# Kernel tuning notes

Hardware: AMD Instinct MI355X
Metric: run time of the kernel (lower is better)

Reference implementation:

```python
import jax, jax.numpy as jnp
import numpy as np


def _seg_softmax(e, seg, n):
    m = jax.ops.segment_max(e, seg, num_segments=n)
    ex = jnp.exp(e - m[seg])
    s = jax.ops.segment_sum(ex, seg, num_segments=n)
    return ex / (s[seg] + 1e-16)


def _gat_conv(x, src, dst, ea, W, a_s, a_d, We, a_e, b, heads, C, concat, N):
    # PyG GATConv math (eval mode, no dropout)
    h = (x @ W).reshape(N, heads, C)                    # [N,H,C]
    he = (ea @ We).reshape(-1, heads, C)                # [Ef,H,C]
    al = jnp.sum(h * a_s, -1)[src] + jnp.sum(h * a_d, -1)[dst] + jnp.sum(he * a_e, -1)
    al = jax.nn.leaky_relu(al, 0.2)                     # [Ef,H]
    alpha = _seg_softmax(al, dst, N)
    out = jax.ops.segment_sum(alpha[:, :, None] * h[src], dst, num_segments=N)
    out = out.reshape(N, heads * C) if concat else out.mean(1)
    return out + b


def _ln(x, g, b):
    mu = x.mean(-1, keepdims=True)
    v = x.var(-1, keepdims=True)
    return (x - mu) / jnp.sqrt(v + 1e-5) * g + b


def setup_inputs() -> dict:
    key = jax.random.key(0)
    ks = jax.random.split(key, 20)
    B, L, E_PER = 512, 64, 4
    N = B * L
    E = N * E_PER
    x = jax.random.normal(ks[0], (N, 55), jnp.float32)
    # within-graph random edges (each graph is a contiguous block of L nodes)
    off = (jnp.arange(E) // (L * E_PER)) * L
    src = off + jax.random.randint(ks[1], (E,), 0, L)
    dst = off + jax.random.randint(ks[2], (E,), 0, L)
    edge_index = jnp.stack([src, dst])
    edge_attr = jax.random.uniform(ks[3], (E, 6), dtype=jnp.float32)
    node_gid = jnp.arange(N) // L
    food_ids = jax.random.randint(ks[4], (B,), 0, 29)
    p = lambda i, shape: jax.random.normal(ks[i], shape, jnp.float32) * 0.05
    return dict(
        x=x, edge_attr=edge_attr, edge_index=edge_index, node_gid=node_gid, food_ids=food_ids,
        W1=p(5, (55, 1024)), as1=p(6, (4, 256)), ad1=p(7, (4, 256)),
        We1=p(8, (6, 1024)), ae1=p(9, (4, 256)), b1=jnp.zeros((1024,), jnp.float32),
        g1=jnp.ones((1024,), jnp.float32), be1=jnp.zeros((1024,), jnp.float32),
        W2=p(10, (1024, 256)), as2=p(11, (1, 256)), ad2=p(12, (1, 256)),
        We2=p(13, (6, 256)), ae2=p(14, (1, 256)), b2=jnp.zeros((256,), jnp.float32),
        g2=jnp.ones((256,), jnp.float32), be2=jnp.zeros((256,), jnp.float32),
        Wa=p(15, (256, 256)), va=p(16, (256,)), emb=p(17, (29, 256)))


def reference(x, edge_attr, edge_index, node_gid, food_ids,
              W1, as1, ad1, We1, ae1, b1, g1, be1,
              W2, as2, ad2, We2, ae2, b2, g2, be2,
              Wa, va, emb):
    N = x.shape[0]
    B = food_ids.shape[0]
    src, dst = edge_index[0], edge_index[1]
    # add self loops; self-loop edge_attr = mean of incoming edge attrs (PyG fill_value='mean')
    ones = jnp.ones((src.shape[0],), x.dtype)
    deg = jax.ops.segment_sum(ones, dst, num_segments=N)
    mean_ea = jax.ops.segment_sum(edge_attr, dst, num_segments=N) / jnp.maximum(deg, 1.0)[:, None]
    loop = jnp.arange(N)
    src_f = jnp.concatenate([src, loop])
    dst_f = jnp.concatenate([dst, loop])
    ea_f = jnp.concatenate([edge_attr, mean_ea], 0)
    # GATEncoder
    h = _gat_conv(x, src_f, dst_f, ea_f, W1, as1, ad1, We1, ae1, b1, 4, 256, True, N)
    h = jax.nn.relu(_ln(h, g1, be1))
    h = _gat_conv(h, src_f, dst_f, ea_f, W2, as2, ad2, We2, ae2, b2, 1, 256, False, N)
    h = _ln(h, g2, be2)                                  # [N,256]
    # per-graph attention over nodes, then attention-weighted max-pool
    scores = jnp.tanh(h @ Wa) @ va                       # [N]
    attn = _seg_softmax(scores, node_gid, B)             # [N]
    hw = h * attn[:, None]
    drug_fea = jax.ops.segment_max(hw, node_gid, num_segments=B)[:, None, :]  # [B,1,256]
    food_fea = emb[food_ids][:, None, :]                 # [B,1,256]
    return drug_fea, food_fea, attn
```

## Files before the change

kernel.cpp:

```cpp
#include <hip/hip_runtime.h>
#include <cstdint>
#include <cstddef>


#define LEAKY_SLOPE 0.2f

typedef __attribute__((ext_vector_type(8))) _Float16 half8;
typedef __attribute__((ext_vector_type(4))) float facc4;

__global__ void k_prep_w(const float* __restrict__ W1, const float* __restrict__ W2,
                         const float* __restrict__ Wa,
                         const float* __restrict__ We1, const float* __restrict__ ae1,
                         const float* __restrict__ We2, const float* __restrict__ ae2,
                         const float* __restrict__ as1, const float* __restrict__ ad1,
                         _Float16* __restrict__ w1t, _Float16* __restrict__ w2t,
                         _Float16* __restrict__ wat, float* __restrict__ fold) {
    int idx = blockIdx.x * blockDim.x + threadIdx.x;
    if (idx < 1024 * 64) {
        int c = idx >> 6, k = idx & 63;
        w1t[idx] = (k < 55) ? (_Float16)W1[(size_t)k * 1024 + c] : (_Float16)0.f;
        return;
    }
    idx -= 1024 * 64;
    if (idx < 256 * 1024) {
        int c = idx >> 10, k = idx & 1023;
        w2t[idx] = (_Float16)W2[(size_t)k * 256 + c];
        return;
    }
    idx -= 256 * 1024;
    if (idx < 256 * 256) {
        int c = idx >> 8, k = idx & 255;
        int dst = ((c >> 4) * 8 + (k >> 5)) * 512 + ((c & 15) + 16 * ((k >> 3) & 3)) * 8 + (k & 7);
        wat[dst] = (_Float16)Wa[(size_t)k * 256 + c];
        return;
    }
    int t = idx - 256 * 256;
    if (t < 24) {
        int k = t >> 2, h = t & 3;
        float s = 0.f;
        for (int c = 0; c < 256; ++c) s += We1[k * 1024 + h * 256 + c] * ae1[h * 256 + c];
        fold[t] = s;
    } else if (t < 30) {
        int k = t - 24;
        float s = 0.f;
        for (int c = 0; c < 256; ++c) s += We2[k * 256 + c] * ae2[c];
        fold[32 + k] = s;
    } else if (t >= 64 && t < 284) {
        int i = t - 64, k = i >> 2, h = i & 3;
        float s = 0.f;
        for (int c = 0; c < 256; ++c) s += W1[k * 1024 + h * 256 + c] * as1[h * 256 + c];
        fold[64 + i] = s;
    } else if (t >= 320 && t < 540) {
        int i = t - 320, k = i >> 2, h = i & 3;
        float s = 0.f;
        for (int c = 0; c < 256; ++c) s += W1[k * 1024 + h * 256 + c] * ad1[h * 256 + c];
        fold[320 + i] = s;
    }
}

__global__ void k_prep_x(const float* __restrict__ x, const float* __restrict__ wa1,
                         const float* __restrict__ wd1, _Float16* __restrict__ xbf,
                         float* __restrict__ ss1, float* __restrict__ sd1, int N) {
    int idx = blockIdx.x * blockDim.x + threadIdx.x;
    if (idx < N * 64) {
        int n = idx >> 6, k = idx & 63;
        _Float16 v = (k < 55) ? (_Float16)x[(size_t)n * 55 + k] : (_Float16)0.f;
        int g = n >> 6, nl = n & 63;
        size_t dst = (size_t)g * 4096 +
                     (((k >> 4) * 2 + (nl >> 5)) * 512 +
                      ((k & 15) + 16 * ((nl >> 3) & 3)) * 8 + (nl & 7));
        xbf[dst] = v;
        return;
    }
    int n = idx - N * 64;
    if (n >= N) return;
    float a0 = 0, a1 = 0, a2 = 0, a3 = 0, d0 = 0, d1 = 0, d2 = 0, d3 = 0;
    for (int k = 0; k < 55; ++k) {
        float xv = x[(size_t)n * 55 + k];
        float4 wa = *reinterpret_cast<const float4*>(&wa1[k * 4]);
        float4 wd = *reinterpret_cast<const float4*>(&wd1[k * 4]);
        a0 += xv * wa.x; a1 += xv * wa.y; a2 += xv * wa.z; a3 += xv * wa.w;
        d0 += xv * wd.x; d1 += xv * wd.y; d2 += xv * wd.z; d3 += xv * wd.w;
    }
    *reinterpret_cast<float4*>(&ss1[n * 4]) = make_float4(a0, a1, a2, a3);
    *reinterpret_cast<float4*>(&sd1[n * 4]) = make_float4(d0, d1, d2, d3);
}

__global__ __launch_bounds__(256) void k_graph_csr(
    const int* __restrict__ ei, const float* __restrict__ ea,
    const float* __restrict__ we1, const float* __restrict__ we2,
    int* __restrict__ coff, int* __restrict__ eid,
    float* __restrict__ ead1, float* __restrict__ ead2, int E, int B) {
    __shared__ int degL[64];
    __shared__ float meaL[64][6];
    __shared__ int cs[65];
    __shared__ int fillL[64];
    int g = blockIdx.x;
    int ng = g * 64;
    int e0 = g * 256;
    int tid = threadIdx.x;
    if (tid < 64) {
        degL[tid] = 0; fillL[tid] = 0;
#pragma unroll
        for (int k = 0; k < 6; ++k) meaL[tid][k] = 0.f;
    }
    __syncthreads();
    int eg = e0 + tid;
    int dst = ei[E + eg];
    int dl = dst - ng;
    atomicAdd(&degL[dl], 1);
#pragma unroll
    for (int k = 0; k < 6; ++k) atomicAdd(&meaL[dl][k], ea[(size_t)eg * 6 + k]);
    __syncthreads();
    if (tid < 64) {
        int v = degL[tid] + 1;
        int incl = v;
#pragma unroll
        for (int o = 1; o < 64; o <<= 1) {
            int up = __shfl_up(incl, o);
            if (tid >= o) incl += up;
        }
        cs[tid + 1] = incl;
        if (tid == 0) cs[0] = 0;
        coff[ng + tid] = g * 320 + (incl - v);
        if (g == B - 1 && tid == 63) coff[ng + 64] = (g + 1) * 320;
    }
    __syncthreads();
    {
        float v[4] = {};
        float v2 = 0.f;
        const float* eap = ea + (size_t)eg * 6;
#pragma unroll
        for (int k = 0; k < 6; ++k) {
            float a = eap[k];
#pragma unroll
            for (int h = 0; h < 4; ++h) v[h] += a * we1[k * 4 + h];
            v2 += a * we2[k];
        }
#pragma unroll
        for (int h = 0; h < 4; ++h) ead1[(size_t)eg * 4 + h] = v[h];
        ead2[eg] = v2;
        int pos = cs[dl] + atomicAdd(&fillL[dl], 1);
        eid[g * 320 + pos] = eg;
    }
    if (tid < 64) {
        float inv = 1.f / fmaxf((float)degL[tid], 1.f);
        float v[4] = {};
        float v2 = 0.f;
#pragma unroll
        for (int k = 0; k < 6; ++k) {
            float a = meaL[tid][k] * inv;
#pragma unroll
            for (int h = 0; h < 4; ++h) v[h] += a * we1[k * 4 + h];
            v2 += a * we2[k];
        }
        int se = E + ng + tid;
#pragma unroll
        for (int h = 0; h < 4; ++h) ead1[(size_t)se * 4 + h] = v[h];
        ead2[se] = v2;
        int pos = cs[tid] + atomicAdd(&fillL[tid], 1);
        eid[g * 320 + pos] = se;
    }
}

__global__ __launch_bounds__(512) void k_pbuild1(
    const _Float16* __restrict__ xbf,
    const int* __restrict__ coff, const int* __restrict__ eid, const int* __restrict__ ei,
    const float* __restrict__ ead1, const float* __restrict__ ss1,
    const float* __restrict__ sd1,
    _Float16* __restrict__ XA, int ldxa, int E, int g0) {
    __shared__ _Float16 Pm[4][64 * 64];
    __shared__ float llds[384][4];
    __shared__ int slds[384];
    int g = blockIdx.x;
    int ng = (g0 + g) * 64;
    int lr0 = g * 64;
    int tid = threadIdx.x;
    int lane = tid & 63, wid = tid >> 6;
    int l15 = lane & 15, l4 = lane >> 4;
    for (int i = tid; i < 4 * 64 * 64 / 8; i += 512)
        *reinterpret_cast<int4*>(&Pm[0][0] + i * 8) = int4{0, 0, 0, 0};
    int pbase = coff[ng];
    int pcnt = coff[ng + 64] - pbase;
    if (pcnt > 384) pcnt = 384;
    for (int p = tid; p < pcnt; p += 512) {
        int e = eid[pbase + p];
        int s, d;
        if (e < E) { s = ei[e]; d = ei[E + e]; } else { s = e - E; d = s; }
        slds[p] = s - ng;
        float4 sv = *reinterpret_cast<const float4*>(&ss1[s * 4]);
        float4 dv = *reinterpret_cast<const float4*>(&sd1[d * 4]);
        float4 ev = *reinterpret_cast<const float4*>(&ead1[(size_t)e * 4]);
        float v0 = sv.x + dv.x + ev.x, v1 = sv.y + dv.y + ev.y;
        float v2 = sv.z + dv.z + ev.z, v3 = sv.w + dv.w + ev.w;
        llds[p][0] = (v0 > 0.f) ? v0 : LEAKY_SLOPE * v0;
        llds[p][1] = (v1 > 0.f) ? v1 : LEAKY_SLOPE * v1;
        llds[p][2] = (v2 > 0.f) ? v2 : LEAKY_SLOPE * v2;
        llds[p][3] = (v3 > 0.f) ? v3 : LEAKY_SLOPE * v3;
    }
    __syncthreads();
    if (tid < 256) {
        int dst = tid >> 2, h = tid & 3;
        int p0 = coff[ng + dst] - pbase, p1 = coff[ng + dst + 1] - pbase;
        float m = -1e30f;
        for (int p = p0; p < p1; ++p) m = fmaxf(m, llds[p][h]);
        float sm = 0.f;
        for (int p = p0; p < p1; ++p) sm += expf(llds[p][h] - m);
        float iv = 1.f / (sm + 1e-16f);
        for (int p = p0; p < p1; ++p) {
            int src = slds[p];
            int pos = dst * 64 + (((src >> 3) ^ (dst & 7)) << 3) + (src & 7);
            Pm[h][pos] = (_Float16)((float)Pm[h][pos] + expf(llds[p][h] - m) * iv);
        }
    }
    __syncthreads();
    int head = wid >> 1, fjh = wid & 1;
    const _Float16* xg = xbf + (size_t)(g0 + g) * 4096;
    facc4 acc[4][2] = {};
#pragma unroll
    for (int kk = 0; kk < 2; ++kk) {
        half8 af[4], bf[2];
#pragma unroll
        for (int f = 0; f < 4; ++f) {
            int arow = f * 16 + l15;
            af[f] = *reinterpret_cast<const half8*>(
                &Pm[head][arow * 64 + (((kk * 4 + l4) ^ (arow & 7)) << 3)]);
        }
#pragma unroll
        for (int f = 0; f < 2; ++f)
            bf[f] = *reinterpret_cast<const half8*>(
                xg + (((fjh * 2 + f) * 2 + kk) * 512 + lane * 8));
#pragma unroll
        for (int fi = 0; fi < 4; ++fi)
#pragma unroll
            for (int fj = 0; fj < 2; ++fj)
                acc[fi][fj] = __builtin_amdgcn_mfma_f32_16x16x32_f16(
                    af[fi], bf[fj], acc[fi][fj], 0, 0, 0);
    }
#pragma unroll
    for (int fi = 0; fi < 4; ++fi)
#pragma unroll
        for (int fj = 0; fj < 2; ++fj)
#pragma unroll
            for (int i = 0; i < 4; ++i) {
                int r = fi * 16 + l4 * 4 + i;
                int k2 = fjh * 32 + fj * 16 + l15;
                XA[((size_t)head * ldxa + lr0 + r) * 64 + k2] = (_Float16)acc[fi][fj][i];
            }
}

__global__ __launch_bounds__(256) void k_gemm_heads(
    const _Float16* __restrict__ XA, int ldxa, const _Float16* __restrict__ w1t,
    _Float16* __restrict__ hpre) {
    int h = blockIdx.z;
    const _Float16* A = XA + (size_t)h * ldxa * 64;
    const _Float16* BT = w1t + (size_t)h * 256 * 64;
    __shared__ _Float16 As[128 * 64];
    __shared__ _Float16 Bs[128 * 64];
    int tid = threadIdx.x;
    int lane = tid & 63, wid = tid >> 6;
    int wr = wid >> 1, wc = wid & 1;
    int l15 = lane & 15, l4 = lane >> 4;
    int r0 = blockIdx.y * 128, c0 = blockIdx.x * 128;
    facc4 acc[4][4] = {};
#pragma unroll
    for (int i = 0; i < 4; ++i) {
        int ch = tid + 256 * i;
        int row = ch >> 3, col16 = ch & 7;
        int sw = col16 ^ (row & 7);
        *reinterpret_cast<int4*>(&As[row * 64 + sw * 8]) =
            *reinterpret_cast<const int4*>(A + (size_t)(r0 + row) * 64 + col16 * 8);
        *reinterpret_cast<int4*>(&Bs[row * 64 + sw * 8]) =
            *reinterpret_cast<const int4*>(BT + (size_t)(c0 + row) * 64 + col16 * 8);
    }
    __syncthreads();
#pragma unroll
    for (int kk = 0; kk < 2; ++kk) {
        half8 af[4], bf[4];
#pragma unroll
        for (int f = 0; f < 4; ++f) {
            int arow = wr * 64 + f * 16 + l15;
            int ac = (kk * 4 + l4) ^ (arow & 7);
            af[f] = *reinterpret_cast<const half8*>(&As[arow * 64 + ac * 8]);
            int brow = wc * 64 + f * 16 + l15;
            int bc = (kk * 4 + l4) ^ (brow & 7);
            bf[f] = *reinterpret_cast<const half8*>(&Bs[brow * 64 + bc * 8]);
        }
#pragma unroll
        for (int fi = 0; fi < 4; ++fi)
#pragma unroll
            for (int fj = 0; fj < 4; ++fj)
                acc[fi][fj] = __builtin_amdgcn_mfma_f32_16x16x32_f16(
                    af[fi], bf[fj], acc[fi][fj], 0, 0, 0);
    }
#pragma unroll
    for (int fi = 0; fi < 4; ++fi)
#pragma unroll
        for (int fj = 0; fj < 4; ++fj)
#pragma unroll
            for (int i = 0; i < 4; ++i) {
                int r = r0 + wr * 64 + fi * 16 + l4 * 4 + i;
                int cc = h * 256 + c0 + wc * 64 + fj * 16 + l15;
                hpre[(size_t)r * 1024 + cc] = (_Float16)acc[fi][fj][i];
            }
}

__global__ __launch_bounds__(256) void k_ln1(
    const _Float16* __restrict__ hpre, const float* __restrict__ b1,
    const float* __restrict__ g1, const float* __restrict__ be1,
    _Float16* __restrict__ hln) {
    int row = blockIdx.x * 4 + (threadIdx.x >> 6);
    int lane = threadIdx.x & 63;
    const _Float16* src = hpre + (size_t)row * 1024;
    float v[16];
    half8 h0 = *reinterpret_cast<const half8*>(src + lane * 8);
    half8 h1 = *reinterpret_cast<const half8*>(src + 512 + lane * 8);
    float lsum = 0.f, lsq = 0.f;
#pragma unroll
    for (int j = 0; j < 8; ++j) {
        v[j] = (float)h0[j] + b1[lane * 8 + j];
        v[8 + j] = (float)h1[j] + b1[512 + lane * 8 + j];
    }
#pragma unroll
    for (int j = 0; j < 16; ++j) { lsum += v[j]; lsq += v[j] * v[j]; }
    for (int o = 32; o; o >>= 1) { lsum += __shfl_xor(lsum, o); lsq += __shfl_xor(lsq, o); }
    float mu = lsum * (1.f / 1024.f);
    float var = lsq * (1.f / 1024.f) - mu * mu;
    float rstd = rsqrtf(var + 1e-5f);
    half8 o0, o1;
#pragma unroll
    for (int j = 0; j < 8; ++j) {
        int c = lane * 8 + j;
        o0[j] = (_Float16)fmaxf((v[j] - mu) * rstd * g1[c] + be1[c], 0.f);
    }
#pragma unroll
    for (int j = 0; j < 8; ++j) {
        int c = 512 + lane * 8 + j;
        o1[j] = (_Float16)fmaxf((v[8 + j] - mu) * rstd * g1[c] + be1[c], 0.f);
    }
    *reinterpret_cast<half8*>(hln + (size_t)row * 1024 + lane * 8) = o0;
    *reinterpret_cast<half8*>(hln + (size_t)row * 1024 + 512 + lane * 8) = o1;
}

__global__ __launch_bounds__(512) void k_gemm2(
    const _Float16* __restrict__ A, const _Float16* __restrict__ BT,
    _Float16* __restrict__ h2f) {
    __shared__ _Float16 As[128 * 64];
    __shared__ _Float16 Bs[256 * 64];
    int tid = threadIdx.x;
    int lane = tid & 63, wid = tid >> 6;
    int wr = wid >> 2, wc = wid & 3;
    int l15 = lane & 15, l4 = lane >> 4;
    int r0 = blockIdx.x * 128;
    facc4 acc[4][4] = {};
    for (int kt = 0; kt < 1024; kt += 64) {
#pragma unroll
        for (int i = 0; i < 2; ++i) {
            int ch = tid + 512 * i;
            int row = ch >> 3, col16 = ch & 7;
            int sw = col16 ^ (row & 7);
            *reinterpret_cast<int4*>(&As[row * 64 + sw * 8]) =
                *reinterpret_cast<const int4*>(A + (size_t)(r0 + row) * 1024 + kt + col16 * 8);
        }
#pragma unroll
        for (int i = 0; i < 4; ++i) {
            int ch = tid + 512 * i;
            int row = ch >> 3, col16 = ch & 7;
            int sw = col16 ^ (row & 7);
            *reinterpret_cast<int4*>(&Bs[row * 64 + sw * 8]) =
                *reinterpret_cast<const int4*>(BT + (size_t)row * 1024 + kt + col16 * 8);
        }
        __syncthreads();
#pragma unroll
        for (int kk = 0; kk < 2; ++kk) {
            half8 af[4], bf[4];
#pragma unroll
            for (int f = 0; f < 4; ++f) {
                int arow = wr * 64 + f * 16 + l15;
                int ac = (kk * 4 + l4) ^ (arow & 7);
                af[f] = *reinterpret_cast<const half8*>(&As[arow * 64 + ac * 8]);
                int brow = wc * 64 + f * 16 + l15;
                int bc = (kk * 4 + l4) ^ (brow & 7);
                bf[f] = *reinterpret_cast<const half8*>(&Bs[brow * 64 + bc * 8]);
            }
#pragma unroll
            for (int fi = 0; fi < 4; ++fi)
#pragma unroll
                for (int fj = 0; fj < 4; ++fj)
                    acc[fi][fj] = __builtin_amdgcn_mfma_f32_16x16x32_f16(
                        af[fi], bf[fj], acc[fi][fj], 0, 0, 0);
        }
        __syncthreads();
    }
#pragma unroll
    for (int fi = 0; fi < 4; ++fi)
#pragma unroll
        for (int fj = 0; fj < 4; ++fj)
#pragma unroll
            for (int i = 0; i < 4; ++i) {
                int r = r0 + wr * 64 + fi * 16 + l4 * 4 + i;
                int cc = wc * 64 + fj * 16 + l15;
                int g = r >> 6, nl = r & 63;
                size_t dst = (size_t)g * 16384 +
                             (((cc >> 4) * 2 + (nl >> 5)) * 512 +
                              ((cc & 15) + 16 * ((nl >> 3) & 3)) * 8 + (nl & 7));
                h2f[dst] = (_Float16)acc[fi][fj][i];
            }
}

__global__ __launch_bounds__(512) void k_graph2(
    const _Float16* __restrict__ h2f,
    const int* __restrict__ coff, const int* __restrict__ eid, const int* __restrict__ ei,
    const float* __restrict__ ead2, const float* __restrict__ as2,
    const float* __restrict__ ad2,
    const float* __restrict__ b2, const float* __restrict__ g2,
    const float* __restrict__ be2,
    float* __restrict__ hfc, _Float16* __restrict__ hfb, int E, int g0) {
    __shared__ _Float16 Pm[64 * 64];
    __shared__ float llds[384];
    __shared__ int slds[384];
    __shared__ float rsum[64], rsq[64], ss2L[64], sd2L[64];
    int g = blockIdx.x;
    int ng = (g0 + g) * 64;
    int lr0 = g * 64;
    int tid = threadIdx.x;
    int lane = tid & 63, wid = tid >> 6;
    int l15 = lane & 15, l4 = lane >> 4;
    int cbase = wid * 32;
    if (tid < 64) { rsum[tid] = 0.f; rsq[tid] = 0.f; ss2L[tid] = 0.f; sd2L[tid] = 0.f; }
    for (int i = tid; i < 64 * 64 / 8; i += 512)
        *reinterpret_cast<int4*>(&Pm[0] + i * 8) = int4{0, 0, 0, 0};
    __syncthreads();
    const _Float16* hg = h2f + (size_t)g * 16384;
    half8 bfr[2][2];
#pragma unroll
    for (int kk = 0; kk < 2; ++kk)
#pragma unroll
        for (int f = 0; f < 2; ++f)
            bfr[kk][f] = *reinterpret_cast<const half8*>(
                hg + ((((cbase + f * 16) >> 4) * 2 + kk) * 512 + lane * 8));
    float ps[2][8] = {}, pd[2][8] = {};
#pragma unroll
    for (int kk = 0; kk < 2; ++kk)
#pragma unroll
        for (int f = 0; f < 2; ++f) {
            int c = cbase + f * 16 + l15;
            float a2 = as2[c], d2 = ad2[c];
#pragma unroll
            for (int j = 0; j < 8; ++j) {
                float hv = (float)bfr[kk][f][j];
                ps[kk][j] += hv * a2;
                pd[kk][j] += hv * d2;
            }
        }
#pragma unroll
    for (int kk = 0; kk < 2; ++kk)
#pragma unroll
        for (int j = 0; j < 8; ++j) {
            float s = ps[kk][j], d = pd[kk][j];
            s += __shfl_xor(s, 1); d += __shfl_xor(d, 1);
            s += __shfl_xor(s, 2); d += __shfl_xor(d, 2);
            s += __shfl_xor(s, 4); d += __shfl_xor(d, 4);
            s += __shfl_xor(s, 8); d += __shfl_xor(d, 8);
            if (l15 == 0) {
                int n = kk * 32 + l4 * 8 + j;
                atomicAdd(&ss2L[n], s);
                atomicAdd(&sd2L[n], d);
            }
        }
    __syncthreads();
    int pbase = coff[ng];
    int pcnt = coff[ng + 64] - pbase;
    if (pcnt > 384) pcnt = 384;
    for (int p = tid; p < pcnt; p += 512) {
        int e = eid[pbase + p];
        int s, d;
        if (e < E) { s = ei[e]; d = ei[E + e]; } else { s = e - E; d = s; }
        slds[p] = s - ng;
        float v = ss2L[s - ng] + sd2L[d - ng] + ead2[e];
        llds[p] = (v > 0.f) ? v : LEAKY_SLOPE * v;
    }
    __syncthreads();
    if (tid < 64) {
        int dst = tid;
        int p0 = coff[ng + dst] - pbase, p1 = coff[ng + dst + 1] - pbase;
        float m = -1e30f;
        for (int p = p0; p < p1; ++p) m = fmaxf(m, llds[p]);
        float sm = 0.f;
        for (int p = p0; p < p1; ++p) sm += expf(llds[p] - m);
        float iv = 1.f / (sm + 1e-16f);
        for (int p = p0; p < p1; ++p) {
            int src = slds[p];
            int pos = dst * 64 + (((src >> 3) ^ (dst & 7)) << 3) + (src & 7);
            Pm[pos] = (_Float16)((float)Pm[pos] + expf(llds[p] - m) * iv);
        }
    }
    __syncthreads();
    facc4 acc[4][2] = {};
#pragma unroll
    for (int kk = 0; kk < 2; ++kk) {
        half8 af[4];
#pragma unroll
        for (int f = 0; f < 4; ++f) {
            int arow = f * 16 + l15;
            af[f] = *reinterpret_cast<const half8*>(
                &Pm[arow * 64 + (((kk * 4 + l4) ^ (arow & 7)) << 3)]);
        }
#pragma unroll
        for (int fi = 0; fi < 4; ++fi)
#pragma unroll
            for (int fj = 0; fj < 2; ++fj)
                acc[fi][fj] = __builtin_amdgcn_mfma_f32_16x16x32_f16(
                    af[fi], bfr[kk][fj], acc[fi][fj], 0, 0, 0);
    }
    float bb[2];
#pragma unroll
    for (int fj = 0; fj < 2; ++fj) bb[fj] = b2[cbase + fj * 16 + l15];
#pragma unroll
    for (int fi = 0; fi < 4; ++fi)
#pragma unroll
        for (int i = 0; i < 4; ++i) {
            float s = 0.f, q = 0.f;
#pragma unroll
            for (int fj = 0; fj < 2; ++fj) {
                float v = acc[fi][fj][i] + bb[fj];
                acc[fi][fj][i] = v;
                s += v; q += v * v;
            }
            s += __shfl_xor(s, 1); q += __shfl_xor(q, 1);
            s += __shfl_xor(s, 2); q += __shfl_xor(q, 2);
            s += __shfl_xor(s, 4); q += __shfl_xor(q, 4);
            s += __shfl_xor(s, 8); q += __shfl_xor(q, 8);
            if (l15 == 0) {
                int r = fi * 16 + l4 * 4 + i;
                atomicAdd(&rsum[r], s);
                atomicAdd(&rsq[r], q);
            }
        }
    __syncthreads();
#pragma unroll
    for (int fi = 0; fi < 4; ++fi)
#pragma unroll
        for (int i = 0; i < 4; ++i) {
            int r = fi * 16 + l4 * 4 + i;
            float mu = rsum[r] * (1.f / 256.f);
            float var = rsq[r] * (1.f / 256.f) - mu * mu;
            float rstd = rsqrtf(var + 1e-5f);
#pragma unroll
            for (int fj = 0; fj < 2; ++fj) {
                int c = cbase + fj * 16 + l15;
                float v = (acc[fi][fj][i] - mu) * rstd * g2[c] + be2[c];
                hfc[(size_t)(lr0 + r) * 256 + c] = v;
                size_t dst = (size_t)g * 16384 +
                             ((fi * 8 + (c >> 5)) * 512 +
                              ((r & 15) + 16 * ((c >> 3) & 3)) * 8 + (c & 7));
                hfb[dst] = (_Float16)v;
            }
        }
}

__global__ __launch_bounds__(512) void k_scores_final(
    const _Float16* __restrict__ hfb, const _Float16* __restrict__ wat,
    const float* __restrict__ va, const float* __restrict__ hfc,
    const int* __restrict__ food, const float* __restrict__ emb,
    float* __restrict__ out, int B, int g0) {
    __shared__ float part[8][64];
    __shared__ float at[64];
    __shared__ float pmax[2][256];
    int g = blockIdx.x;
    int b = g0 + g;
    int r0 = g * 64;
    int tid = threadIdx.x;
    int lane = tid & 63, wid = tid >> 6;
    int l15 = lane & 15, l4 = lane >> 4;
    int cbase = wid * 32;
    const _Float16* hg = hfb + (size_t)g * 16384;
    facc4 acc[4][2] = {};
#pragma unroll
    for (int kk = 0; kk < 8; ++kk) {
        half8 af[4], bf[2];
#pragma unroll
        for (int f = 0; f < 4; ++f)
            af[f] = *reinterpret_cast<const half8*>(hg + ((f * 8 + kk) * 512 + lane * 8));
#pragma unroll
        for (int f = 0; f < 2; ++f)
            bf[f] = *reinterpret_cast<const half8*>(
                wat + (((wid * 2 + f) * 8 + kk) * 512 + lane * 8));
#pragma unroll
        for (int fi = 0; fi < 4; ++fi)
#pragma unroll
            for (int fj = 0; fj < 2; ++fj)
                acc[fi][fj] = __builtin_amdgcn_mfma_f32_16x16x32_f16(
                    af[fi], bf[fj], acc[fi][fj], 0, 0, 0);
    }
    float vac[2];
#pragma unroll
    for (int fj = 0; fj < 2; ++fj) vac[fj] = va[cbase + fj * 16 + l15];
#pragma unroll
    for (int fi = 0; fi < 4; ++fi)
#pragma unroll
        for (int i = 0; i < 4; ++i) {
            float v = tanhf(acc[fi][0][i]) * vac[0] + tanhf(acc[fi][1][i]) * vac[1];
            v += __shfl_xor(v, 1); v += __shfl_xor(v, 2);
            v += __shfl_xor(v, 4); v += __shfl_xor(v, 8);
            if (l15 == 0) part[wid][fi * 16 + l4 * 4 + i] = v;
        }
    __syncthreads();
    if (tid < 64) {
        float sc = part[0][tid] + part[1][tid] + part[2][tid] + part[3][tid] +
                   part[4][tid] + part[5][tid] + part[6][tid] + part[7][tid];
        float m = sc;
        for (int o = 32; o; o >>= 1) m = fmaxf(m, __shfl_xor(m, o));
        float ex = expf(sc - m);
        float s = ex;
        for (int o = 32; o; o >>= 1) s += __shfl_xor(s, o);
        float a = ex / (s + 1e-16f);
        at[tid] = a;
        out[(size_t)B * 512 + (size_t)b * 64 + tid] = a;
    }
    __syncthreads();
    {
        int c = tid & 255, half = tid >> 8;
        float m = -1e30f;
        for (int l = half * 32; l < half * 32 + 32; ++l)
            m = fmaxf(m, hfc[(size_t)(r0 + l) * 256 + c] * at[l]);
        pmax[half][c] = m;
    }
    __syncthreads();
    if (tid < 256) {
        out[(size_t)b * 256 + tid] = fmaxf(pmax[0][tid], pmax[1][tid]);
        out[(size_t)B * 256 + (size_t)b * 256 + tid] =
            emb[(size_t)food[b] * 256 + tid];
    }
}

extern "C" void kernel_launch(void* const* d_in, const int* in_sizes, int n_in,
                              void* d_out, int out_size, void* d_ws, size_t ws_size,
                              hipStream_t stream) {
    const float* x   = (const float*)d_in[0];
    const float* ea  = (const float*)d_in[1];
    const int*   ei  = (const int*)d_in[2];
    const int*   food= (const int*)d_in[4];
    const float* W1  = (const float*)d_in[5];
    const float* as1 = (const float*)d_in[6];
    const float* ad1 = (const float*)d_in[7];
    const float* We1 = (const float*)d_in[8];
    const float* ae1 = (const float*)d_in[9];
    const float* b1  = (const float*)d_in[10];
    const float* g1  = (const float*)d_in[11];
    const float* be1 = (const float*)d_in[12];
    const float* W2  = (const float*)d_in[13];
    const float* as2 = (const float*)d_in[14];
    const float* ad2 = (const float*)d_in[15];
    const float* We2 = (const float*)d_in[16];
    const float* ae2 = (const float*)d_in[17];
    const float* b2  = (const float*)d_in[18];
    const float* g2  = (const float*)d_in[19];
    const float* be2 = (const float*)d_in[20];
    const float* Wa  = (const float*)d_in[21];
    const float* va  = (const float*)d_in[22];
    const float* emb = (const float*)d_in[23];
    float* out = (float*)d_out;

    const int N  = in_sizes[0] / 55;
    const int E  = in_sizes[2] / 2;
    const int B  = in_sizes[4];
    const int Ef = E + N;
    const int LPG = N / B;

    char* w = (char*)d_ws;
    size_t off = 0;
    auto take = [&](size_t bytes) -> char* {
        char* p = w + off;
        off = (off + bytes + 255) & ~(size_t)255;
        return p;
    };
    int*      coff = (int*)take((size_t)(N + 1) * 4);
    int*      eid  = (int*)take((size_t)Ef * 4);
    float*    ead1 = (float*)take((size_t)Ef * 4 * 4);
    float*    ead2 = (float*)take((size_t)Ef * 4);
    float*    fold = (float*)take(4096 * 4);
    float*    ss1  = (float*)take((size_t)N * 4 * 4);
    float*    sd1  = (float*)take((size_t)N * 4 * 4);
    _Float16* xbf  = (_Float16*)take((size_t)N * 64 * 2);
    _Float16* w1t  = (_Float16*)take((size_t)1024 * 64 * 2);
    _Float16* w2t  = (_Float16*)take((size_t)256 * 1024 * 2);
    _Float16* wat  = (_Float16*)take((size_t)256 * 256 * 2);
    size_t smallEnd = off;

    int G = B;
    while (G > 2 && smallEnd + (size_t)G * 32768 + 2ull * G * 131072 + 768 > ws_size) G >>= 1;
    _Float16* XA   = (_Float16*)take((size_t)G * 32768);
    _Float16* hpre = (_Float16*)take((size_t)G * 131072);
    _Float16* hln  = (_Float16*)take((size_t)G * 131072);
    _Float16* h2f = (_Float16*)hpre;
    float*    hfc = (float*)((char*)hpre + (size_t)G * 32768);
    _Float16* hfb = (_Float16*)((char*)hpre + (size_t)G * 98304);

    k_prep_w<<<(1024 * 64 + 256 * 1024 + 256 * 256 + 3072 + 255) / 256, 256, 0, stream>>>(
        W1, W2, Wa, We1, ae1, We2, ae2, as1, ad1, w1t, w2t, wat, fold);
    k_prep_x<<<(N * 64 + N + 255) / 256, 256, 0, stream>>>(
        x, fold + 64, fold + 320, xbf, ss1, sd1, N);
    k_graph_csr<<<B, 256, 0, stream>>>(ei, ea, fold, fold + 32, coff, eid,
                                       ead1, ead2, E, B);

    for (int g0 = 0; g0 < B; g0 += G) {
        int Gc = (g0 + G <= B) ? G : (B - g0);
        int n0 = g0 * LPG;
        (void)n0;
        int NC = Gc * LPG;
        k_pbuild1<<<Gc, 512, 0, stream>>>(xbf, coff, eid, ei, ead1, ss1, sd1,
                                          XA, NC, E, g0);
        k_gemm_heads<<<dim3(2, NC / 128, 4), 256, 0, stream>>>(XA, NC, w1t, hpre);
        k_ln1<<<NC / 4, 256, 0, stream>>>(hpre, b1, g1, be1, hln);
        k_gemm2<<<NC / 128, 512, 0, stream>>>(hln, w2t, h2f);
        k_graph2<<<Gc, 512, 0, stream>>>(h2f, coff, eid, ei, ead2, as2, ad2,
                                         b2, g2, be2, hfc, hfb, E, g0);
        k_scores_final<<<Gc, 512, 0, stream>>>(hfb, wat, va, hfc, food, emb,
                                               out, B, g0);
    }
}
```

Measured before the change: 163.1 us.

## Fuse second GAT layer with attention scoring and pooling kernel

Merges k_graph2 and k_scores_final into one kernel per graph. The layer-norm output stays in LDS as an fp16 MFMA-ready tile and in registers as fp32, instead of being written to global hfc/hfb and read back. The attention-weighted max-pool now reduces straight from registers with cross-lane shuffles. This removes one launch and a global round trip of the per-graph features, at the cost of more LDS and register pressure in a single 512-thread block.

```diff
diff --git a/kernel.cpp b/kernel.cpp
--- a/kernel.cpp
+++ b/kernel.cpp
@@ -408,21 +408,26 @@
             }
 }
 
-__global__ __launch_bounds__(512) void k_graph2(
+__global__ __launch_bounds__(512) void k_graph2f(
     const _Float16* __restrict__ h2f,
     const int* __restrict__ coff, const int* __restrict__ eid, const int* __restrict__ ei,
     const float* __restrict__ ead2, const float* __restrict__ as2,
     const float* __restrict__ ad2,
     const float* __restrict__ b2, const float* __restrict__ g2,
     const float* __restrict__ be2,
-    float* __restrict__ hfc, _Float16* __restrict__ hfb, int E, int g0) {
-    __shared__ _Float16 Pm[64 * 64];
-    __shared__ float llds[384];
-    __shared__ int slds[384];
+    const _Float16* __restrict__ wat, const float* __restrict__ va,
+    const int* __restrict__ food, const float* __restrict__ emb,
+    float* __restrict__ out, int E, int B, int g0) {
+    __shared__ _Float16 hfL[64 * 256];
+    _Float16* Pm = hfL;
+    float* llds = reinterpret_cast<float*>(hfL + 4096);
+    int* slds = reinterpret_cast<int*>(hfL + 4096 + 768);
     __shared__ float rsum[64], rsq[64], ss2L[64], sd2L[64];
+    __shared__ float part[8][64];
+    __shared__ float at[64];
     int g = blockIdx.x;
+    int b = g0 + g;
     int ng = (g0 + g) * 64;
-    int lr0 = g * 64;
     int tid = threadIdx.x;
     int lane = tid & 63, wid = tid >> 6;
     int l15 = lane & 15, l4 = lane >> 4;
@@ -542,46 +547,28 @@
     for (int fi = 0; fi < 4; ++fi)
 #pragma unroll
         for (int i = 0; i < 4; ++i) {
-            int r = fi * 16 + l4 * 4 + i;
-            float mu = rsum[r] * (1.f / 256.f);
-            float var = rsq[r] * (1.f / 256.f) - mu * mu;
+            int rl = l4 * 4 + i;
+            float mu = rsum[fi * 16 + rl] * (1.f / 256.f);
+            float var = rsq[fi * 16 + rl] * (1.f / 256.f) - mu * mu;
             float rstd = rsqrtf(var + 1e-5f);
 #pragma unroll
             for (int fj = 0; fj < 2; ++fj) {
                 int c = cbase + fj * 16 + l15;
                 float v = (acc[fi][fj][i] - mu) * rstd * g2[c] + be2[c];
-                hfc[(size_t)(lr0 + r) * 256 + c] = v;
-                size_t dst = (size_t)g * 16384 +
-                             ((fi * 8 + (c >> 5)) * 512 +
-                              ((r & 15) + 16 * ((c >> 3) & 3)) * 8 + (c & 7));
-                hfb[dst] = (_Float16)v;
-            }
-        }
-}
-
-__global__ __launch_bounds__(512) void k_scores_final(
-    const _Float16* __restrict__ hfb, const _Float16* __restrict__ wat,
-    const float* __restrict__ va, const float* __restrict__ hfc,
-    const int* __restrict__ food, const float* __restrict__ emb,
-    float* __restrict__ out, int B, int g0) {
-    __shared__ float part[8][64];
-    __shared__ float at[64];
-    __shared__ float pmax[2][256];
-    int g = blockIdx.x;
-    int b = g0 + g;
-    int r0 = g * 64;
-    int tid = threadIdx.x;
-    int lane = tid & 63, wid = tid >> 6;
-    int l15 = lane & 15, l4 = lane >> 4;
-    int cbase = wid * 32;
-    const _Float16* hg = hfb + (size_t)g * 16384;
-    facc4 acc[4][2] = {};
+                acc[fi][fj][i] = v;
+                int idx = (fi * 8 + wid) * 512 +
+                          ((fj * 2 + (l15 >> 3)) * 16 + rl) * 8 + (l15 & 7);
+                hfL[idx] = (_Float16)v;
+            }
+        }
+    __syncthreads();
+    facc4 acc2[4][2] = {};
 #pragma unroll
     for (int kk = 0; kk < 8; ++kk) {
         half8 af[4], bf[2];
 #pragma unroll
         for (int f = 0; f < 4; ++f)
-            af[f] = *reinterpret_cast<const half8*>(hg + ((f * 8 + kk) * 512 + lane * 8));
+            af[f] = *reinterpret_cast<const half8*>(&hfL[(f * 8 + kk) * 512 + lane * 8]);
 #pragma unroll
         for (int f = 0; f < 2; ++f)
             bf[f] = *reinterpret_cast<const half8*>(
@@ -590,8 +577,8 @@
         for (int fi = 0; fi < 4; ++fi)
 #pragma unroll
             for (int fj = 0; fj < 2; ++fj)
-                acc[fi][fj] = __builtin_amdgcn_mfma_f32_16x16x32_f16(
-                    af[fi], bf[fj], acc[fi][fj], 0, 0, 0);
+                acc2[fi][fj] = __builtin_amdgcn_mfma_f32_16x16x32_f16(
+                    af[fi], bf[fj], acc2[fi][fj], 0, 0, 0);
     }
     float vac[2];
 #pragma unroll
@@ -600,7 +587,7 @@
     for (int fi = 0; fi < 4; ++fi)
 #pragma unroll
         for (int i = 0; i < 4; ++i) {
-            float v = tanhf(acc[fi][0][i]) * vac[0] + tanhf(acc[fi][1][i]) * vac[1];
+            float v = tanhf(acc2[fi][0][i]) * vac[0] + tanhf(acc2[fi][1][i]) * vac[1];
             v += __shfl_xor(v, 1); v += __shfl_xor(v, 2);
             v += __shfl_xor(v, 4); v += __shfl_xor(v, 8);
             if (l15 == 0) part[wid][fi * 16 + l4 * 4 + i] = v;
@@ -619,19 +606,24 @@
         out[(size_t)B * 512 + (size_t)b * 64 + tid] = a;
     }
     __syncthreads();
-    {
-        int c = tid & 255, half = tid >> 8;
+#pragma unroll
+    for (int fj = 0; fj < 2; ++fj) {
         float m = -1e30f;
-        for (int l = half * 32; l < half * 32 + 32; ++l)
-            m = fmaxf(m, hfc[(size_t)(r0 + l) * 256 + c] * at[l]);
-        pmax[half][c] = m;
-    }
-    __syncthreads();
-    if (tid < 256) {
-        out[(size_t)b * 256 + tid] = fmaxf(pmax[0][tid], pmax[1][tid]);
+#pragma unroll
+        for (int fi = 0; fi < 4; ++fi)
+#pragma unroll
+            for (int i = 0; i < 4; ++i) {
+                int r = fi * 16 + l4 * 4 + i;
+                m = fmaxf(m, acc[fi][fj][i] * at[r]);
+            }
+        m = fmaxf(m, __shfl_xor(m, 16));
+        m = fmaxf(m, __shfl_xor(m, 32));
+        if (l4 == 0)
+            out[(size_t)b * 256 + cbase + fj * 16 + l15] = m;
+    }
+    if (tid < 256)
         out[(size_t)B * 256 + (size_t)b * 256 + tid] =
             emb[(size_t)food[b] * 256 + tid];
-    }
 }
 
 extern "C" void kernel_launch(void* const* d_in, const int* in_sizes, int n_in,
@@ -693,9 +685,7 @@
     _Float16* XA   = (_Float16*)take((size_t)G * 32768);
     _Float16* hpre = (_Float16*)take((size_t)G * 131072);
     _Float16* hln  = (_Float16*)take((size_t)G * 131072);
-    _Float16* h2f = (_Float16*)hpre;
-    float*    hfc = (float*)((char*)hpre + (size_t)G * 32768);
-    _Float16* hfb = (_Float16*)((char*)hpre + (size_t)G * 98304);
+    _Float16* h2f  = (_Float16*)hpre;
 
     k_prep_w<<<(1024 * 64 + 256 * 1024 + 256 * 256 + 3072 + 255) / 256, 256, 0, stream>>>(
         W1, W2, Wa, We1, ae1, We2, ae2, as1, ad1, w1t, w2t, wat, fold);
@@ -706,17 +696,14 @@
 
     for (int g0 = 0; g0 < B; g0 += G) {
         int Gc = (g0 + G <= B) ? G : (B - g0);
-        int n0 = g0 * LPG;
-        (void)n0;
         int NC = Gc * LPG;
         k_pbuild1<<<Gc, 512, 0, stream>>>(xbf, coff, eid, ei, ead1, ss1, sd1,
                                           XA, NC, E, g0);
         k_gemm_heads<<<dim3(2, NC / 128, 4), 256, 0, stream>>>(XA, NC, w1t, hpre);
         k_ln1<<<NC / 4, 256, 0, stream>>>(hpre, b1, g1, be1, hln);
         k_gemm2<<<NC / 128, 512, 0, stream>>>(hln, w2t, h2f);
-        k_graph2<<<Gc, 512, 0, stream>>>(h2f, coff, eid, ei, ead2, as2, ad2,
-                                         b2, g2, be2, hfc, hfb, E, g0);
-        k_scores_final<<<Gc, 512, 0, stream>>>(hfb, wat, va, hfc, food, emb,
-                                               out, B, g0);
-    }
-}
+        k_graph2f<<<Gc, 512, 0, stream>>>(h2f, coff, eid, ei, ead2, as2, ad2,
+                                          b2, g2, be2, wat, va, food, emb,
+                                          out, E, B, g0);
+    }
+}
```

Result: faster. 150.8 us, median of 2 (-7.5%).
